# Performance work log

Measured on AMD Instinct MI355X. Metric: run time of the kernel, lower is better.

Reference implementation:

```python
import jax, jax.numpy as jnp
import numpy as np

L = 4        # num_layers
N = 50000    # nodes
E = 500000   # edges
B = 32       # graphs
H = 64       # hidden_dim
HP = 16      # hidden_dim_pe
P = 8        # pe_dim
BN_EPS = 1e-5


def setup_inputs() -> dict:
    key = jax.random.key(0)
    ks = jax.random.split(key, 22)
    nrm = lambda k, s: jax.random.normal(k, s, dtype=jnp.float32)
    w = lambda k, s: nrm(k, s) * 0.1
    return {
        'x': nrm(ks[0], (N, H)),
        'pe': nrm(ks[1], (N, P)),
        'Lambda': jax.random.uniform(ks[2], (B, P), dtype=jnp.float32),
        'edge_attr': nrm(ks[3], (E, H)),
        'edge_index': jax.random.randint(ks[4], (2, E), 0, N),
        'batch': jnp.sort(jax.random.randint(ks[5], (N,), 0, B)),
        # edge encoder (SPE): eigenvalue MLP + output projection
        'We1': w(ks[6], (L, P, HP * P)), 'be1': jnp.zeros((L, HP * P)),
        'Wee': w(ks[7], (L, HP, H)),     'bee': jnp.zeros((L, H)),
        # GINE mlp: Linear-BN-ReLU-Linear
        'W1': w(ks[8], (L, H, H)), 'b1': jnp.zeros((L, H)),
        'g1': jnp.ones((L, H)),    'beta1': jnp.zeros((L, H)),
        'W2': w(ks[9], (L, H, H)), 'b2': jnp.zeros((L, H)),
        # equivariant PE conv: edge gate + channel Linear
        'Wg': w(ks[10], (L, H, HP)),  'bg': jnp.zeros((L, HP)),
        'Wp': w(ks[11], (L, HP, HP)), 'bp': jnp.zeros((L, HP)),
        # outer BatchNorm per layer
        'gn': jnp.ones((L, H)), 'bnb': jnp.zeros((L, H)),
    }


def _bn(h, gamma, beta):
    mu = h.mean(0)
    var = h.var(0)
    return gamma * (h - mu) * jax.lax.rsqrt(var + BN_EPS) + beta


def reference(x, pe, Lambda, edge_attr, We1, be1, Wee, bee, W1, b1, g1, beta1,
              W2, b2, Wg, bg, Wp, bp, gn, bnb, edge_index, batch):
    src, dst = edge_index[0], edge_index[1]
    bsrc = batch[src]                       # [E] graph id of source node
    z = jnp.tile(pe[:, None, :], (1, HP, 1))  # [N, HP, P]
    for i in range(L):
        # SPE edge encoder: phi(Lambda)-weighted inner product over pe axis
        phi = jax.nn.relu(Lambda @ We1[i] + be1[i]).reshape(B, HP, P)
        eh = jnp.einsum('ehp,ehp->eh', phi[bsrc] * z[src], z[dst])  # [E, HP]
        ea = eh @ Wee[i] + bee[i] + edge_attr                       # [E, H]
        # GINEConv: scatter-add of relu(x_src + edge_attr), eps = 0
        agg = jax.ops.segment_sum(jax.nn.relu(x[src] + ea), dst, num_segments=N)
        h = x + agg
        h = jax.nn.relu(_bn(h @ W1[i] + b1[i], g1[i], beta1[i])) @ W2[i] + b2[i]
        # GINConvEquivariant: gated scatter-add, Linear on channel axis
        gate = jax.nn.relu(ea @ Wg[i] + bg[i])                      # [E, HP]
        msgz = jax.nn.relu(z[src] + gate[:, :, None])               # [E, HP, P]
        z = z + jax.ops.segment_sum(msgz, dst, num_segments=N)
        z = jnp.einsum('nhp,hk->nkp', z, Wp[i]) + bp[i][None, :, None]
        x = _bn(h, gn[i], bnb[i])
        if i != L - 1:
            x = jax.nn.relu(x)
    return x, z
```

## Files before the change

kernel.cpp:

```cpp
#include <hip/hip_runtime.h>

#define NN 50000
#define EE 500000
#define LL 4

typedef unsigned short u16;
typedef unsigned int u32;

__device__ __forceinline__ float bfc(u16 u) { return __uint_as_float(((u32)u) << 16); }
__device__ __forceinline__ u16 f2bf(float f) {
    u32 u = __float_as_uint(f);
    return (u16)((u + 0x7fffu + ((u >> 16) & 1u)) >> 16);
}
__device__ __forceinline__ float lanebc(float v, int l) {
    return __int_as_float(__builtin_amdgcn_readlane(__float_as_int(v), l));
}
__device__ __forceinline__ void unpack2(u32 w, float& lo, float& hi) {
    lo = __uint_as_float(w << 16);
    hi = __uint_as_float(w & 0xffff0000u);
}

__global__ __launch_bounds__(256) void k_init(const float* __restrict__ x, float* __restrict__ Xf,
                                              u16* __restrict__ Xh, int big,
                                              int* __restrict__ deg, int* __restrict__ cursor) {
    for (int i = blockIdx.x * 256 + threadIdx.x; i < NN * 64; i += gridDim.x * 256) {
        if (big) Xh[i] = f2bf(x[i]);
        else Xf[i] = x[i];
    }
    for (int i = blockIdx.x * 256 + threadIdx.x; i < NN; i += gridDim.x * 256) {
        deg[i] = 0;
        cursor[i] = 0;
    }
}

__global__ __launch_bounds__(128) void k_phi(const float* __restrict__ Lam, const float* __restrict__ We1,
                                             const float* __restrict__ be1, float* __restrict__ phiA) {
    int l = blockIdx.x >> 5, b = blockIdx.x & 31, j = threadIdx.x;
    float acc = be1[l * 128 + j];
    for (int q = 0; q < 8; q++)
        acc = fmaf(Lam[b * 8 + q], We1[l * 1024 + q * 128 + j], acc);
    phiA[l * 4096 + b * 128 + j] = fmaxf(acc, 0.f);
}

__global__ __launch_bounds__(256) void k_small(const float* __restrict__ Wee, const float* __restrict__ Wg,
                                               float* __restrict__ MA) {
    int l = blockIdx.x, t = threadIdx.x;
    int k = t >> 4, h = t & 15;
    float m = 0.f;
    for (int f = 0; f < 64; f++)
        m = fmaf(Wee[l * 1024 + k * 64 + f], Wg[l * 1024 + f * 16 + h], m);
    MA[l * 256 + t] = m;
}

__global__ __launch_bounds__(256) void k_hist(const int* __restrict__ ei, int* __restrict__ deg) {
    int e = blockIdx.x * 256 + threadIdx.x;
    if (e < EE) {
        int d = ei[EE + e];
        if (d >= 0 && d < NN) atomicAdd(&deg[d], 1);
    }
}

__global__ __launch_bounds__(256) void k_scan1(const int* __restrict__ deg, int* __restrict__ rowptr,
                                               int* __restrict__ bsum) {
    __shared__ int tmp[256];
    int t = threadIdx.x, i = blockIdx.x * 256 + t;
    int v = (i < NN) ? deg[i] : 0;
    tmp[t] = v;
    __syncthreads();
    for (int off = 1; off < 256; off <<= 1) {
        int a = (t >= off) ? tmp[t - off] : 0;
        __syncthreads();
        tmp[t] += a;
        __syncthreads();
    }
    if (i < NN) rowptr[i] = tmp[t] - v;
    if (t == 255) bsum[blockIdx.x] = tmp[255];
}

__global__ __launch_bounds__(256) void k_scan2(const int* __restrict__ bsum, int* __restrict__ boff,
                                               int* __restrict__ rowptr, int nb) {
    __shared__ int tmp[256];
    int t = threadIdx.x;
    int v = (t < nb) ? bsum[t] : 0;
    tmp[t] = v;
    __syncthreads();
    for (int off = 1; off < 256; off <<= 1) {
        int a = (t >= off) ? tmp[t - off] : 0;
        __syncthreads();
        tmp[t] += a;
        __syncthreads();
    }
    if (t < nb) boff[t] = tmp[t] - v;
    if (t == 255) rowptr[NN] = tmp[255];
}

__global__ __launch_bounds__(256) void k_scan3(int* __restrict__ rowptr, const int* __restrict__ boff) {
    int i = blockIdx.x * 256 + threadIdx.x;
    if (i < NN) rowptr[i] += boff[blockIdx.x];
}

__global__ __launch_bounds__(256) void k_scatter(const int* __restrict__ ei, const int* __restrict__ batch,
                                                 const int* __restrict__ rowptr, int* __restrict__ cursor,
                                                 u32* __restrict__ sb, int* __restrict__ eeo) {
    int e = blockIdx.x * 256 + threadIdx.x;
    if (e < EE) {
        int s = ei[e], d = ei[EE + e];
        if (s < 0) s = 0; if (s >= NN) s = NN - 1;
        if (d < 0) d = 0; if (d >= NN) d = NN - 1;
        int pos = rowptr[d] + atomicAdd(&cursor[d], 1);
        if (pos >= 0 && pos < EE) {
            sb[pos] = (u32)s | ((u32)(batch[s] & 31) << 16);
            eeo[pos] = e;
        }
    }
}

__global__ __launch_bounds__(256) void k_perm(const float* __restrict__ eat, const int* __restrict__ eeo,
                                              u16* __restrict__ eatp) {
    const float4* e4 = reinterpret_cast<const float4*>(eat);
    ushort4* o4 = reinterpret_cast<ushort4*>(eatp);
    for (long long i = (long long)blockIdx.x * 256 + threadIdx.x; i < (long long)EE * 16;
         i += (long long)gridDim.x * 256) {
        int idx = (int)(i >> 4), cc = (int)(i & 15);
        int e = eeo[idx];
        float4 v = e4[(size_t)e * 16 + cc];
        ushort4 o;
        o.x = f2bf(v.x); o.y = f2bf(v.y); o.z = f2bf(v.z); o.w = f2bf(v.w);
        o4[i] = o;
    }
}

__global__ __launch_bounds__(256) void k_eag2(const u16* __restrict__ eatp, const float* __restrict__ WgL,
                                              const float* __restrict__ beeL, const float* __restrict__ bgL,
                                              u32* __restrict__ EAGp) {
    __shared__ float sWg[1024];
    __shared__ float scv[16];
    __shared__ u32 srow[256][33];
    const int t = threadIdx.x;
    for (int i = t; i < 1024; i += 256) sWg[i] = WgL[i];
    __syncthreads();
    if (t < 16) {
        float c = bgL[t];
        for (int j = 0; j < 64; j++) c = fmaf(beeL[j], sWg[j * 16 + t], c);
        scv[t] = c;
    }
    const int base = blockIdx.x * 256;
    const u32* eat32 = (const u32*)eatp;
    for (int i = t; i < 256 * 32; i += 256) {
        int r = i >> 5, c = i & 31;
        int idx = base + r;
        srow[r][c] = (idx < EE) ? eat32[(size_t)idx * 32 + c] : 0u;
    }
    __syncthreads();
    const int idx = base + t;
    if (idx < EE) {
        float acc[16];
#pragma unroll
        for (int h = 0; h < 16; h++) acc[h] = scv[h];
#pragma unroll
        for (int c = 0; c < 32; c++) {
            float a0, a1;
            unpack2(srow[t][c], a0, a1);
            const float* w0 = &sWg[(2 * c) * 16];
#pragma unroll
            for (int h = 0; h < 16; h++) acc[h] = fmaf(a0, w0[h], fmaf(a1, w0[16 + h], acc[h]));
        }
        u32 w[8];
#pragma unroll
        for (int h = 0; h < 8; h++) w[h] = (u32)f2bf(acc[h]) | ((u32)f2bf(acc[8 + h]) << 16);
        uint4* op = reinterpret_cast<uint4*>(EAGp + (size_t)idx * 8);
        op[0] = make_uint4(w[0], w[1], w[2], w[3]);
        op[1] = make_uint4(w[4], w[5], w[6], w[7]);
    }
}

#define EF(P, kk) do { \
    P##w = (u32)__builtin_amdgcn_readlane((int)svec, (kk)); \
    int s_ = (int)(P##w & 0xffffu); \
    if (INM == 0) { P##z0 = P##z1 = pe[s_ * 8 + pp]; } \
    else { float2 t_ = Z2[s_ * 64 + lane]; P##z0 = t_.x; P##z1 = t_.y; } \
    P##xs = bfc(Xh[s_ * 64 + lane]); \
    size_t ge_ = (size_t)(c + (kk)); \
    P##ea = bfc(eatp[ge_ * 64 + lane]); \
    unpack2(EAGp[ge_ * 8 + hlo], P##gl, P##gh); \
} while (0)

#define EC(P, MSK) do { \
    int b_ = (int)((P##w >> 16) & 31u); \
    float p0 = sphi[b_ * 128 + lane] * P##z0 * zd0; \
    float p1 = sphi[b_ * 128 + 64 + lane] * P##z1 * zd1; \
    p0 += __shfl_xor(p0, 1); p1 += __shfl_xor(p1, 1); \
    p0 += __shfl_xor(p0, 2); p1 += __shfl_xor(p1, 2); \
    p0 += __shfl_xor(p0, 4); p1 += __shfl_xor(p1, 4); \
    float eaA = 0.f, eaB = 0.f, gA = P##gl, gB = 0.f, hA = P##gh, hB = 0.f; \
    _Pragma("unroll") \
    for (int k_ = 0; k_ < 8; k_++) { float e_ = lanebc(p0, k_ << 3); \
        eaA = fmaf(e_, wee[k_], eaA); gA = fmaf(e_, mlo[k_], gA); hA = fmaf(e_, mhi[k_], hA); } \
    _Pragma("unroll") \
    for (int k_ = 0; k_ < 8; k_++) { float e_ = lanebc(p1, k_ << 3); \
        eaB = fmaf(e_, wee[8 + k_], eaB); gB = fmaf(e_, mlo[8 + k_], gB); hB = fmaf(e_, mhi[8 + k_], hB); } \
    float ea_ = beev + P##ea + eaA + eaB; \
    accx = fmaf(MSK, fmaxf(0.f, P##xs + ea_), accx); \
    az0  = fmaf(MSK, fmaxf(0.f, P##z0 + fmaxf(gA + gB, 0.f)), az0); \
    az1  = fmaf(MSK, fmaxf(0.f, P##z1 + fmaxf(hA + hB, 0.f)), az1); \
} while (0)

template <int INM, int FIN>
__global__ __launch_bounds__(256) void k_edge2(const float2* __restrict__ Z2,
                                               const float* __restrict__ pe,
                                               const u16* __restrict__ Xh,
                                               const u16* __restrict__ eatp, const u32* __restrict__ EAGp,
                                               const int* __restrict__ rowptr, const u32* __restrict__ sb,
                                               const float* __restrict__ phiL, const float* __restrict__ WeeL,
                                               const float* __restrict__ beeL, const float* __restrict__ ML,
                                               const float* __restrict__ WpL, const float* __restrict__ bpL,
                                               float* __restrict__ Hf, float2* __restrict__ Z2O,
                                               float* __restrict__ outz,
                                               double* __restrict__ stats) {
    __shared__ float sphi[4096];
    __shared__ float sWp[256];
    __shared__ float sbp[16];
    if (blockIdx.x == 0) stats[threadIdx.x] = 0.0;
    for (int t = threadIdx.x; t < 4096; t += 256) sphi[t] = phiL[t];
    if (threadIdx.x < 256) sWp[threadIdx.x] = WpL[threadIdx.x];
    if (threadIdx.x < 16) sbp[threadIdx.x] = bpL[threadIdx.x];
    const int lane = threadIdx.x & 63;
    const int wid = threadIdx.x >> 6;
    const int hlo = lane >> 3;
    const int pp = lane & 7;
    float wee[16], mlo[16], mhi[16];
#pragma unroll
    for (int k = 0; k < 16; k++) {
        wee[k] = WeeL[k * 64 + lane];
        mlo[k] = ML[k * 16 + hlo];
        mhi[k] = ML[k * 16 + 8 + hlo];
    }
    const float beev = beeL[lane];
    __syncthreads();
    for (int n = blockIdx.x * 4 + wid; n < NN; n += gridDim.x * 4) {
        float zd0, zd1;
        if (INM == 0) { zd0 = zd1 = pe[n * 8 + pp]; }
        else { float2 t = Z2[n * 64 + lane]; zd0 = t.x; zd1 = t.y; }
        float accx = bfc(Xh[n * 64 + lane]);
        float az0 = zd0, az1 = zd1;
        int i0 = rowptr[n], i1 = rowptr[n + 1];
        if (i0 < 0) i0 = 0;
        if (i1 > EE) i1 = EE;
        for (int c = i0; c < i1; c += 64) {
            const int ce = (c + 64 < i1) ? c + 64 : i1;
            const int m = ce - c;
            const int mL = m - 1;
            int ci = c + lane; if (ci > i1 - 1) ci = i1 - 1;
            const u32 svec = sb[ci];
            u32 Aw, Bw, Nw, Mw;
            float Az0, Az1, Axs, Aea, Agl, Agh;
            float Bz0, Bz1, Bxs, Bea, Bgl, Bgh;
            float Nz0, Nz1, Nxs, Nea, Ngl, Ngh;
            float Mz0, Mz1, Mxs, Mea, Mgl, Mgh;
            EF(A, 0);
            EF(B, (1 > mL ? mL : 1));
            for (int k = 0; k < m; k += 2) {
                const int n0 = (k + 2 > mL) ? mL : k + 2;
                const int n1 = (k + 3 > mL) ? mL : k + 3;
                EF(N, n0);
                EF(M, n1);
                EC(A, 1.f);
                EC(B, (k + 1 <= mL) ? 1.f : 0.f);
                Aw = Nw; Az0 = Nz0; Az1 = Nz1; Axs = Nxs; Aea = Nea; Agl = Ngl; Agh = Ngh;
                Bw = Mw; Bz0 = Mz0; Bz1 = Mz1; Bxs = Mxs; Bea = Mea; Bgl = Mgl; Bgh = Mgh;
            }
        }
        Hf[n * 64 + lane] = accx;
        float r0 = sbp[hlo], r1 = sbp[8 + hlo];
#pragma unroll
        for (int h = 0; h < 8; h++) {
            const float v = __shfl(az0, (h << 3) + pp);
            r0 = fmaf(v, sWp[h * 16 + hlo], r0);
            r1 = fmaf(v, sWp[h * 16 + 8 + hlo], r1);
        }
#pragma unroll
        for (int h = 0; h < 8; h++) {
            const float v = __shfl(az1, (h << 3) + pp);
            r0 = fmaf(v, sWp[(8 + h) * 16 + hlo], r0);
            r1 = fmaf(v, sWp[(8 + h) * 16 + 8 + hlo], r1);
        }
        if (FIN) {
            outz[n * 128 + lane] = r0;
            outz[n * 128 + 64 + lane] = r1;
        } else {
            Z2O[n * 64 + lane] = make_float2(r0, r1);
        }
    }
}

template <int INM>
__global__ __launch_bounds__(256) void k_edge_s(const float* __restrict__ Zf,
                                                const float* __restrict__ pe,
                                                const float* __restrict__ Xf, const float* __restrict__ eat,
                                                const int* __restrict__ rowptr, const u32* __restrict__ sb,
                                                const int* __restrict__ eeo,
                                                const float* __restrict__ phiL, const float* __restrict__ WeeL,
                                                const float* __restrict__ beeL,
                                                const float* __restrict__ WgL, const float* __restrict__ bgL,
                                                const float* __restrict__ WpL, const float* __restrict__ bpL,
                                                float* __restrict__ Hf, float* __restrict__ ZfO,
                                                double* __restrict__ stats) {
    __shared__ float sphi[32 * 128];
    __shared__ float sWp[256];
    __shared__ float sbp[16];
    if (blockIdx.x == 0) stats[threadIdx.x] = 0.0;
    for (int t = threadIdx.x; t < 4096; t += 256) sphi[t] = phiL[t];
    if (threadIdx.x < 256) sWp[threadIdx.x] = WpL[threadIdx.x];
    if (threadIdx.x < 16) sbp[threadIdx.x] = bpL[threadIdx.x];
    const int lane = threadIdx.x & 63;
    const int wid = threadIdx.x >> 6;
    const int hlo = lane >> 3;
    const int pp = lane & 7;
    const int h16 = lane & 15;
    const int g16 = lane & 48;
    float wee[16], wgr[16];
#pragma unroll
    for (int k = 0; k < 16; k++) {
        wee[k] = WeeL[k * 64 + lane];
        wgr[k] = WgL[(g16 + k) * 16 + h16];
    }
    const float beev = beeL[lane];
    const float bgr = bgL[h16];
    __syncthreads();
    for (int n = blockIdx.x * 4 + wid; n < NN; n += gridDim.x * 4) {
        float zd0, zd1;
        if (INM == 0) { zd0 = zd1 = pe[n * 8 + pp]; }
        else { zd0 = Zf[n * 128 + lane]; zd1 = Zf[n * 128 + 64 + lane]; }
        float accx = Xf[n * 64 + lane];
        float az0 = zd0, az1 = zd1;
        int i0 = rowptr[n], i1 = rowptr[n + 1];
        if (i0 < 0) i0 = 0;
        if (i1 > EE) i1 = EE;
        for (int idx = i0; idx < i1; ++idx) {
            const u32 w = sb[idx];
            const int s = w & 0xffff;
            const int b = (w >> 16) & 31;
            int e = eeo[idx];
            e = (e < 0) ? 0 : ((e >= EE) ? EE - 1 : e);
            float zs0, zs1;
            if (INM == 0) { zs0 = zs1 = pe[s * 8 + pp]; }
            else { zs0 = Zf[s * 128 + lane]; zs1 = Zf[s * 128 + 64 + lane]; }
            float p0 = sphi[b * 128 + lane] * zs0 * zd0;
            float p1 = sphi[b * 128 + 64 + lane] * zs1 * zd1;
            p0 += __shfl_xor(p0, 1); p1 += __shfl_xor(p1, 1);
            p0 += __shfl_xor(p0, 2); p1 += __shfl_xor(p1, 2);
            p0 += __shfl_xor(p0, 4); p1 += __shfl_xor(p1, 4);
            float ea = beev + eat[(size_t)e * 64 + lane];
#pragma unroll
            for (int k = 0; k < 8; k++) ea = fmaf(lanebc(p0, k << 3), wee[k], ea);
#pragma unroll
            for (int k = 0; k < 8; k++) ea = fmaf(lanebc(p1, k << 3), wee[8 + k], ea);
            float gp = 0.f;
#pragma unroll
            for (int i = 0; i < 16; i++) gp = fmaf(__shfl(ea, g16 + i), wgr[i], gp);
            gp += __shfl_xor(gp, 16);
            gp += __shfl_xor(gp, 32);
            const float gv = fmaxf(gp + bgr, 0.f);
            const float glo = __shfl(gv, hlo);
            const float ghi = __shfl(gv, 8 + hlo);
            const float xs = Xf[s * 64 + lane];
            accx += fmaxf(0.f, xs + ea);
            az0 += fmaxf(0.f, zs0 + glo);
            az1 += fmaxf(0.f, zs1 + ghi);
        }
        Hf[n * 64 + lane] = accx;
        float r0 = sbp[hlo], r1 = sbp[8 + hlo];
#pragma unroll
        for (int h = 0; h < 8; h++) {
            const float v = __shfl(az0, (h << 3) + pp);
            r0 = fmaf(v, sWp[h * 16 + hlo], r0);
            r1 = fmaf(v, sWp[h * 16 + 8 + hlo], r1);
        }
#pragma unroll
        for (int h = 0; h < 8; h++) {
            const float v = __shfl(az1, (h << 3) + pp);
            r0 = fmaf(v, sWp[(8 + h) * 16 + hlo], r0);
            r1 = fmaf(v, sWp[(8 + h) * 16 + 8 + hlo], r1);
        }
        ZfO[n * 128 + lane] = r0;
        ZfO[n * 128 + 64 + lane] = r1;
    }
}

__global__ __launch_bounds__(256) void k_gemm1(float* Buf, const float* __restrict__ WL,
                                               const float* __restrict__ bL,
                                               double* __restrict__ sum, double* __restrict__ sq) {
    __shared__ float sW[4096];
    __shared__ double red[512];
    for (int t = threadIdx.x; t < 4096; t += 256) sW[t] = WL[t];
    const int lane = threadIdx.x & 63, wid = threadIdx.x >> 6;
    const float bv = bL[lane];
    __syncthreads();
    double s = 0.0, q = 0.0;
    for (int n = blockIdx.x * 4 + wid; n < NN; n += gridDim.x * 4) {
        const float h = Buf[n * 64 + lane];
        float a0 = bv, a1 = 0.f;
#pragma unroll
        for (int k = 0; k < 32; k++) a0 = fmaf(lanebc(h, k), sW[k * 64 + lane], a0);
#pragma unroll
        for (int k = 32; k < 64; k++) a1 = fmaf(lanebc(h, k), sW[k * 64 + lane], a1);
        const float acc = a0 + a1;
        Buf[n * 64 + lane] = acc;
        s += (double)acc;
        q += (double)acc * (double)acc;
    }
    red[threadIdx.x] = s;
    red[256 + threadIdx.x] = q;
    __syncthreads();
    if (threadIdx.x < 64) {
        s = red[threadIdx.x] + red[threadIdx.x + 64] + red[threadIdx.x + 128] + red[threadIdx.x + 192];
        q = red[256 + threadIdx.x] + red[320 + threadIdx.x] + red[384 + threadIdx.x] + red[448 + threadIdx.x];
        atomicAdd(&sum[lane], s);
        atomicAdd(&sq[lane], q);
    }
}

__global__ __launch_bounds__(256) void k_gemm2(float* Buf, const float* __restrict__ WL,
                                               const float* __restrict__ bL,
                                               const float* __restrict__ gL, const float* __restrict__ betaL,
                                               const double* __restrict__ s1, const double* __restrict__ q1,
                                               double* __restrict__ sum, double* __restrict__ sq) {
    __shared__ float sW[4096];
    __shared__ double red[512];
    for (int t = threadIdx.x; t < 4096; t += 256) sW[t] = WL[t];
    const int lane = threadIdx.x & 63, wid = threadIdx.x >> 6;
    const float bv = bL[lane];
    const double mu = s1[lane] * (1.0 / NN);
    const double var = q1[lane] * (1.0 / NN) - mu * mu;
    const float inv = rsqrtf(fmaxf((float)var, 0.f) + 1e-5f);
    const float gm = gL[lane] * inv;
    const float ga = betaL[lane] - (float)mu * gm;
    __syncthreads();
    double s = 0.0, q = 0.0;
    for (int n = blockIdx.x * 4 + wid; n < NN; n += gridDim.x * 4) {
        const float v = Buf[n * 64 + lane];
        const float r = fmaxf(fmaf(v, gm, ga), 0.f);
        float a0 = bv, a1 = 0.f;
#pragma unroll
        for (int k = 0; k < 32; k++) a0 = fmaf(lanebc(r, k), sW[k * 64 + lane], a0);
#pragma unroll
        for (int k = 32; k < 64; k++) a1 = fmaf(lanebc(r, k), sW[k * 64 + lane], a1);
        const float acc = a0 + a1;
        Buf[n * 64 + lane] = acc;
        s += (double)acc;
        q += (double)acc * (double)acc;
    }
    red[threadIdx.x] = s;
    red[256 + threadIdx.x] = q;
    __syncthreads();
    if (threadIdx.x < 64) {
        s = red[threadIdx.x] + red[threadIdx.x + 64] + red[threadIdx.x + 128] + red[threadIdx.x + 192];
        q = red[256 + threadIdx.x] + red[320 + threadIdx.x] + red[384 + threadIdx.x] + red[448 + threadIdx.x];
        atomicAdd(&sum[lane], s);
        atomicAdd(&sq[lane], q);
    }
}

__global__ __launch_bounds__(256) void k_bnout2(const float* __restrict__ In, u16* __restrict__ Xh,
                                                float* __restrict__ outx,
                                                const double* __restrict__ s2, const double* __restrict__ q2,
                                                const float* __restrict__ gL, const float* __restrict__ bL,
                                                int last) {
    int i = blockIdx.x * 256 + threadIdx.x;
    const int f = i & 63;
    const double mu = s2[f] * (1.0 / NN);
    const double var = q2[f] * (1.0 / NN) - mu * mu;
    const float inv = rsqrtf(fmaxf((float)var, 0.f) + 1e-5f);
    const float gm = gL[f] * inv;
    const float ga = bL[f] - (float)mu * gm;
    for (; i < NN * 64; i += gridDim.x * 256) {
        float o = fmaf(In[i], gm, ga);
        if (last) {
            outx[i] = o;
        } else {
            o = fmaxf(o, 0.f);
            Xh[i] = f2bf(o);
        }
    }
}

__global__ __launch_bounds__(256) void k_bnout(const float* __restrict__ In, float* __restrict__ Xf,
                                               const double* __restrict__ s2, const double* __restrict__ q2,
                                               const float* __restrict__ gL, const float* __restrict__ bL,
                                               int dorelu) {
    int i = blockIdx.x * 256 + threadIdx.x;
    const int f = i & 63;
    const double mu = s2[f] * (1.0 / NN);
    const double var = q2[f] * (1.0 / NN) - mu * mu;
    const float inv = rsqrtf(fmaxf((float)var, 0.f) + 1e-5f);
    const float gm = gL[f] * inv;
    const float ga = bL[f] - (float)mu * gm;
    for (; i < NN * 64; i += gridDim.x * 256) {
        float o = fmaf(In[i], gm, ga);
        if (dorelu) o = fmaxf(o, 0.f);
        Xf[i] = o;
    }
}

extern "C" void kernel_launch(void* const* d_in, const int* in_sizes, int n_in,
                              void* d_out, int out_size, void* d_ws, size_t ws_size,
                              hipStream_t stream) {
    (void)in_sizes; (void)n_in; (void)out_size;
    const float* x    = (const float*)d_in[0];
    const float* pe   = (const float*)d_in[1];
    const float* Lam  = (const float*)d_in[2];
    const float* eat  = (const float*)d_in[3];
    const int*   ei   = (const int*)d_in[4];
    const int*   batch= (const int*)d_in[5];
    const float* We1  = (const float*)d_in[6];
    const float* be1  = (const float*)d_in[7];
    const float* Wee  = (const float*)d_in[8];
    const float* bee  = (const float*)d_in[9];
    const float* W1   = (const float*)d_in[10];
    const float* b1   = (const float*)d_in[11];
    const float* g1   = (const float*)d_in[12];
    const float* bt1  = (const float*)d_in[13];
    const float* W2   = (const float*)d_in[14];
    const float* b2   = (const float*)d_in[15];
    const float* Wg   = (const float*)d_in[16];
    const float* bg   = (const float*)d_in[17];
    const float* Wp   = (const float*)d_in[18];
    const float* bp   = (const float*)d_in[19];
    const float* gn   = (const float*)d_in[20];
    const float* bnb  = (const float*)d_in[21];

    float* Xf   = (float*)d_out;
    u16*   Xh   = (u16*)d_out;
    float* B    = (float*)d_out + 3200000;

    float* A    = (float*)d_ws;
    float* Hf   = A + 6400000;
    float* MA   = Hf + 3200000;
    float* phiA = MA + 1024;
    double* stats = (double*)(phiA + 16384);
    double* s1 = stats, *q1 = stats + 64, *s2 = stats + 128, *q2 = stats + 192;
    int* rowptr = (int*)(stats + 256);
    int* deg    = rowptr + NN + 1;
    int* bsum   = deg + NN;
    int* boff   = bsum + 256;
    int* cursor = boff + 256;
    u32* sb     = (u32*)(cursor + NN);
    int* eeo    = (int*)(sb + EE);
    u32* EAGp   = (u32*)(eeo + EE);
    u16* eatp   = (u16*)(EAGp + (size_t)EE * 8);
    const size_t NEED_BIG = (size_t)((char*)(eatp + (size_t)EE * 64) - (char*)d_ws);
    const bool big = (ws_size >= NEED_BIG);

    float2* A2 = (float2*)A;
    float2* B2 = (float2*)B;

    const int NB_N = (NN + 255) / 256;
    const int NB_E = (EE + 255) / 256;

    k_init<<<1024, 256, 0, stream>>>(x, Xf, Xh, big ? 1 : 0, deg, cursor);
    k_phi<<<LL * 32, 128, 0, stream>>>(Lam, We1, be1, phiA);
    k_hist<<<NB_E, 256, 0, stream>>>(ei, deg);
    k_scan1<<<NB_N, 256, 0, stream>>>(deg, rowptr, bsum);
    k_scan2<<<1, 256, 0, stream>>>(bsum, boff, rowptr, NB_N);
    k_scan3<<<NB_N, 256, 0, stream>>>(rowptr, boff);
    k_scatter<<<NB_E, 256, 0, stream>>>(ei, batch, rowptr, cursor, sb, eeo);
    if (big) {
        k_small<<<LL, 256, 0, stream>>>(Wee, Wg, MA);
        k_perm<<<4096, 256, 0, stream>>>(eat, eeo, eatp);
    }

    for (int l = 0; l < LL; l++) {
        const float* WeeL = Wee + l * 1024;
        const float* beeL = bee + l * 64;
        const float* WgL  = Wg + l * 1024;
        const float* bgL  = bg + l * 16;
        const float* WpL  = Wp + l * 256;
        const float* bpL  = bp + l * 16;
        const float* phiL = phiA + l * 4096;
        const float* ML   = MA + l * 256;
        if (big) {
            k_eag2<<<NB_E, 256, 0, stream>>>(eatp, WgL, beeL, bgL, EAGp);
            if (l == 0)
                k_edge2<0, 0><<<6272, 256, 0, stream>>>(A2, pe, Xh, eatp, EAGp, rowptr, sb,
                                                        phiL, WeeL, beeL, ML, WpL, bpL,
                                                        Hf, A2, nullptr, stats);
            else if (l == 1)
                k_edge2<1, 0><<<6272, 256, 0, stream>>>(A2, pe, Xh, eatp, EAGp, rowptr, sb,
                                                        phiL, WeeL, beeL, ML, WpL, bpL,
                                                        Hf, B2, nullptr, stats);
            else if (l == 2)
                k_edge2<1, 0><<<6272, 256, 0, stream>>>(B2, pe, Xh, eatp, EAGp, rowptr, sb,
                                                        phiL, WeeL, beeL, ML, WpL, bpL,
                                                        Hf, A2, nullptr, stats);
            else
                k_edge2<1, 1><<<6272, 256, 0, stream>>>(A2, pe, Xh, eatp, EAGp, rowptr, sb,
                                                        phiL, WeeL, beeL, ML, WpL, bpL,
                                                        Hf, nullptr, B, stats);
        } else {
            const float* Zin  = (l == 2) ? B : A;
            float*       Zout = (l == 1 || l == 3) ? B : A;
            if (l == 0)
                k_edge_s<0><<<2048, 256, 0, stream>>>(nullptr, pe, Xf, eat, rowptr, sb, eeo,
                                                      phiL, WeeL, beeL, WgL, bgL, WpL, bpL,
                                                      Hf, Zout, stats);
            else
                k_edge_s<1><<<2048, 256, 0, stream>>>(Zin, pe, Xf, eat, rowptr, sb, eeo,
                                                      phiL, WeeL, beeL, WgL, bgL, WpL, bpL,
                                                      Hf, Zout, stats);
        }
        k_gemm1<<<512, 256, 0, stream>>>(Hf, W1 + l * 4096, b1 + l * 64, s1, q1);
        k_gemm2<<<512, 256, 0, stream>>>(Hf, W2 + l * 4096, b2 + l * 64,
                                         g1 + l * 64, bt1 + l * 64, s1, q1, s2, q2);
        if (big)
            k_bnout2<<<1024, 256, 0, stream>>>(Hf, Xh, Xf, s2, q2, gn + l * 64, bnb + l * 64,
                                               (l == LL - 1) ? 1 : 0);
        else
            k_bnout<<<1024, 256, 0, stream>>>(Hf, Xf, s2, q2, gn + l * 64, bnb + l * 64,
                                              (l == LL - 1) ? 0 : 1);
    }
}
```

Measured before the change: 1.117 ms.

## Precompute all-layer edge gates in one pass and deduplicate gate matvec across lanes

New measurement: 1.195 ms. 7.0% more time.

```diff
diff --git a/kernel.cpp b/kernel.cpp
--- a/kernel.cpp
+++ b/kernel.cpp
@@ -130,6 +130,54 @@
     }
 }
 
+__global__ __launch_bounds__(256) void k_eag_all(const u16* __restrict__ eatp, const float* __restrict__ Wg,
+                                                 const float* __restrict__ bee, const float* __restrict__ bg,
+                                                 u32* __restrict__ EAGp4) {
+    __shared__ float sWg[4096];
+    __shared__ float scv[64];
+    __shared__ u32 srow[256][33];
+    const int t = threadIdx.x;
+    for (int i = t; i < 4096; i += 256) sWg[i] = Wg[i];
+    __syncthreads();
+    if (t < 64) {
+        const int l = t >> 4, h = t & 15;
+        float c = bg[l * 16 + h];
+        for (int j = 0; j < 64; j++) c = fmaf(bee[l * 64 + j], sWg[l * 1024 + j * 16 + h], c);
+        scv[t] = c;
+    }
+    const int base = blockIdx.x * 256;
+    const u32* eat32 = (const u32*)eatp;
+    for (int i = t; i < 256 * 32; i += 256) {
+        int r = i >> 5, c = i & 31;
+        int idx = base + r;
+        srow[r][c] = (idx < EE) ? eat32[(size_t)idx * 32 + c] : 0u;
+    }
+    __syncthreads();
+    const int idx = base + t;
+    if (idx >= EE) return;
+#pragma unroll
+    for (int l = 0; l < LL; l++) {
+        const float* wl = &sWg[l * 1024];
+        float acc[16];
+#pragma unroll
+        for (int h = 0; h < 16; h++) acc[h] = scv[l * 16 + h];
+#pragma unroll
+        for (int c = 0; c < 32; c++) {
+            float a0, a1;
+            unpack2(srow[t][c], a0, a1);
+            const float* w0 = &wl[(2 * c) * 16];
+#pragma unroll
+            for (int h = 0; h < 16; h++) acc[h] = fmaf(a0, w0[h], fmaf(a1, w0[16 + h], acc[h]));
+        }
+        u32 w[8];
+#pragma unroll
+        for (int h = 0; h < 8; h++) w[h] = (u32)f2bf(acc[h]) | ((u32)f2bf(acc[8 + h]) << 16);
+        uint4* op = reinterpret_cast<uint4*>(EAGp4 + (size_t)l * EE * 8 + (size_t)idx * 8);
+        op[0] = make_uint4(w[0], w[1], w[2], w[3]);
+        op[1] = make_uint4(w[4], w[5], w[6], w[7]);
+    }
+}
+
 __global__ __launch_bounds__(256) void k_eag2(const u16* __restrict__ eatp, const float* __restrict__ WgL,
                                               const float* __restrict__ beeL, const float* __restrict__ bgL,
                                               u32* __restrict__ EAGp) {
@@ -180,9 +228,9 @@
     if (INM == 0) { P##z0 = P##z1 = pe[s_ * 8 + pp]; } \
     else { float2 t_ = Z2[s_ * 64 + lane]; P##z0 = t_.x; P##z1 = t_.y; } \
     P##xs = bfc(Xh[s_ * 64 + lane]); \
-    size_t ge_ = (size_t)(c + (kk)); \
-    P##ea = bfc(eatp[ge_ * 64 + lane]); \
-    unpack2(EAGp[ge_ * 8 + hlo], P##gl, P##gh); \
+    int ge_ = c + (kk); \
+    P##ea = bfc(eatp[(size_t)ge_ * 64 + lane]); \
+    P##gg = EAGp[(size_t)ge_ * 8 + h8]; \
 } while (0)
 
 #define EC(P, MSK) do { \
@@ -192,21 +240,27 @@
     p0 += __shfl_xor(p0, 1); p1 += __shfl_xor(p1, 1); \
     p0 += __shfl_xor(p0, 2); p1 += __shfl_xor(p1, 2); \
     p0 += __shfl_xor(p0, 4); p1 += __shfl_xor(p1, 4); \
-    float eaA = 0.f, eaB = 0.f, gA = P##gl, gB = 0.f, hA = P##gh, hB = 0.f; \
+    float eaA = 0.f, eaB = 0.f, gvA = 0.f, gvB = 0.f; \
     _Pragma("unroll") \
     for (int k_ = 0; k_ < 8; k_++) { float e_ = lanebc(p0, k_ << 3); \
-        eaA = fmaf(e_, wee[k_], eaA); gA = fmaf(e_, mlo[k_], gA); hA = fmaf(e_, mhi[k_], hA); } \
+        eaA = fmaf(e_, wee[k_], eaA); gvA = fmaf(e_, mgr[k_], gvA); } \
     _Pragma("unroll") \
     for (int k_ = 0; k_ < 8; k_++) { float e_ = lanebc(p1, k_ << 3); \
-        eaB = fmaf(e_, wee[8 + k_], eaB); gB = fmaf(e_, mlo[8 + k_], gB); hB = fmaf(e_, mhi[8 + k_], hB); } \
-    float ea_ = beev + P##ea + eaA + eaB; \
+        eaB = fmaf(e_, wee[8 + k_], eaB); gvB = fmaf(e_, mgr[8 + k_], gvB); } \
+    float gl_, gh_; \
+    unpack2(P##gg, gl_, gh_); \
+    const float gval = (lane & 8) ? gh_ : gl_; \
+    const float gv = fmaxf(gval + gvA + gvB, 0.f); \
+    const float glo = __shfl(gv, hlo); \
+    const float ghi = __shfl(gv, 8 + hlo); \
+    const float ea_ = beev + P##ea + eaA + eaB; \
     accx = fmaf(MSK, fmaxf(0.f, P##xs + ea_), accx); \
-    az0  = fmaf(MSK, fmaxf(0.f, P##z0 + fmaxf(gA + gB, 0.f)), az0); \
-    az1  = fmaf(MSK, fmaxf(0.f, P##z1 + fmaxf(hA + hB, 0.f)), az1); \
+    az0  = fmaf(MSK, fmaxf(0.f, P##z0 + glo), az0); \
+    az1  = fmaf(MSK, fmaxf(0.f, P##z1 + ghi), az1); \
 } while (0)
 
 template <int INM, int FIN>
-__global__ __launch_bounds__(256) void k_edge2(const float2* __restrict__ Z2,
+__global__ __launch_bounds__(256) void k_edge3(const float2* __restrict__ Z2,
                                                const float* __restrict__ pe,
                                                const u16* __restrict__ Xh,
                                                const u16* __restrict__ eatp, const u32* __restrict__ EAGp,
@@ -228,12 +282,13 @@
     const int wid = threadIdx.x >> 6;
     const int hlo = lane >> 3;
     const int pp = lane & 7;
-    float wee[16], mlo[16], mhi[16];
+    const int h8 = lane & 7;
+    const int h16 = lane & 15;
+    float wee[16], mgr[16];
 #pragma unroll
     for (int k = 0; k < 16; k++) {
         wee[k] = WeeL[k * 64 + lane];
-        mlo[k] = ML[k * 16 + hlo];
-        mhi[k] = ML[k * 16 + 8 + hlo];
+        mgr[k] = ML[k * 16 + h16];
     }
     const float beev = beeL[lane];
     __syncthreads();
@@ -252,11 +307,11 @@
             const int mL = m - 1;
             int ci = c + lane; if (ci > i1 - 1) ci = i1 - 1;
             const u32 svec = sb[ci];
-            u32 Aw, Bw, Nw, Mw;
-            float Az0, Az1, Axs, Aea, Agl, Agh;
-            float Bz0, Bz1, Bxs, Bea, Bgl, Bgh;
-            float Nz0, Nz1, Nxs, Nea, Ngl, Ngh;
-            float Mz0, Mz1, Mxs, Mea, Mgl, Mgh;
+            u32 Aw, Bw, Nw, Mw, Agg, Bgg, Ngg, Mgg;
+            float Az0, Az1, Axs, Aea;
+            float Bz0, Bz1, Bxs, Bea;
+            float Nz0, Nz1, Nxs, Nea;
+            float Mz0, Mz1, Mxs, Mea;
             EF(A, 0);
             EF(B, (1 > mL ? mL : 1));
             for (int k = 0; k < m; k += 2) {
@@ -266,8 +321,8 @@
                 EF(M, n1);
                 EC(A, 1.f);
                 EC(B, (k + 1 <= mL) ? 1.f : 0.f);
-                Aw = Nw; Az0 = Nz0; Az1 = Nz1; Axs = Nxs; Aea = Nea; Agl = Ngl; Agh = Ngh;
-                Bw = Mw; Bz0 = Mz0; Bz1 = Mz1; Bxs = Mxs; Bea = Mea; Bgl = Mgl; Bgh = Mgh;
+                Aw = Nw; Az0 = Nz0; Az1 = Nz1; Axs = Nxs; Aea = Nea; Agg = Ngg;
+                Bw = Mw; Bz0 = Mz0; Bz1 = Mz1; Bxs = Mxs; Bea = Mea; Bgg = Mgg;
             }
         }
         Hf[n * 64 + lane] = accx;
@@ -546,10 +601,12 @@
     int* cursor = boff + 256;
     u32* sb     = (u32*)(cursor + NN);
     int* eeo    = (int*)(sb + EE);
-    u32* EAGp   = (u32*)(eeo + EE);
-    u16* eatp   = (u16*)(EAGp + (size_t)EE * 8);
-    const size_t NEED_BIG = (size_t)((char*)(eatp + (size_t)EE * 64) - (char*)d_ws);
-    const bool big = (ws_size >= NEED_BIG);
+    u16* eatp   = (u16*)(eeo + EE);
+    u32* EAGp   = (u32*)(eatp + (size_t)EE * 64);
+    const size_t NEED_BIG  = (size_t)((char*)(EAGp + (size_t)EE * 8) - (char*)d_ws);
+    const size_t NEED_BIG2 = (size_t)((char*)(EAGp + (size_t)EE * 32) - (char*)d_ws);
+    const bool big2 = (ws_size >= NEED_BIG2);
+    const bool big  = (ws_size >= NEED_BIG);
 
     float2* A2 = (float2*)A;
     float2* B2 = (float2*)B;
@@ -567,6 +624,8 @@
     if (big) {
         k_small<<<LL, 256, 0, stream>>>(Wee, Wg, MA);
         k_perm<<<4096, 256, 0, stream>>>(eat, eeo, eatp);
+        if (big2)
+            k_eag_all<<<NB_E, 256, 0, stream>>>(eatp, Wg, bee, bg, EAGp);
     }
 
     for (int l = 0; l < LL; l++) {
@@ -579,21 +638,23 @@
         const float* phiL = phiA + l * 4096;
         const float* ML   = MA + l * 256;
         if (big) {
-            k_eag2<<<NB_E, 256, 0, stream>>>(eatp, WgL, beeL, bgL, EAGp);
+            const u32* EAGl = big2 ? (EAGp + (size_t)l * EE * 8) : EAGp;
+            if (!big2)
+                k_eag2<<<NB_E, 256, 0, stream>>>(eatp, WgL, beeL, bgL, EAGp);
             if (l == 0)
-                k_edge2<0, 0><<<6272, 256, 0, stream>>>(A2, pe, Xh, eatp, EAGp, rowptr, sb,
+                k_edge3<0, 0><<<6272, 256, 0, stream>>>(A2, pe, Xh, eatp, EAGl, rowptr, sb,
                                                         phiL, WeeL, beeL, ML, WpL, bpL,
                                                         Hf, A2, nullptr, stats);
             else if (l == 1)
-                k_edge2<1, 0><<<6272, 256, 0, stream>>>(A2, pe, Xh, eatp, EAGp, rowptr, sb,
+                k_edge3<1, 0><<<6272, 256, 0, stream>>>(A2, pe, Xh, eatp, EAGl, rowptr, sb,
                                                         phiL, WeeL, beeL, ML, WpL, bpL,
                                                         Hf, B2, nullptr, stats);
             else if (l == 2)
-                k_edge2<1, 0><<<6272, 256, 0, stream>>>(B2, pe, Xh, eatp, EAGp, rowptr, sb,
+                k_edge3<1, 0><<<6272, 256, 0, stream>>>(B2, pe, Xh, eatp, EAGl, rowptr, sb,
                                                         phiL, WeeL, beeL, ML, WpL, bpL,
                                                         Hf, A2, nullptr, stats);
             else
-                k_edge2<1, 1><<<6272, 256, 0, stream>>>(A2, pe, Xh, eatp, EAGp, rowptr, sb,
+                k_edge3<1, 1><<<6272, 256, 0, stream>>>(A2, pe, Xh, eatp, EAGl, rowptr, sb,
                                                         phiL, WeeL, beeL, ML, WpL, bpL,
                                                         Hf, nullptr, B, stats);
         } else {
```
